# Performance work log

Hardware: AMD Instinct MI355X
Metric: run time of the kernel (lower is better)

## Reference

```python
import jax, jax.numpy as jnp
import numpy as np

NUM_HEADS = 16
EPS = 1e-05


def setup_inputs() -> dict:
    key = jax.random.key(0)
    k1, k2, k3 = jax.random.split(key, 3)
    b, n, d = 2, 2048, 1024
    x = jax.random.normal(k1, (b, n, d), dtype=jnp.float32)
    # nn.Linear weights stored here as (in, out); scaled like typical init
    wqkv = jax.random.normal(k2, (d, 3 * d), dtype=jnp.float32) * (1.0 / np.sqrt(d))
    wo = jax.random.normal(k3, (d, d), dtype=jnp.float32) * (1.0 / np.sqrt(d))
    return {"x": x, "wqkv": wqkv, "wo": wo}


def reference(x, wqkv, wo):
    b, n, d = x.shape
    h = NUM_HEADS
    hd = d // h
    qkv = x @ wqkv                      # (b, n, 3d)
    q, k, v = jnp.split(qkv, 3, axis=-1)
    q = jax.nn.relu(q)
    k = jax.nn.relu(k)
    # (b, n, h*hd) -> (b, h, n, hd)
    split_heads = lambda t: t.reshape(b, n, h, hd).transpose(0, 2, 1, 3)
    q, k, v = split_heads(q), split_heads(k), split_heads(v)
    # cumulative outer products: kv[b,h,t] = sum_{s<=t} k_s (x) v_s  -> (b,h,n,hd,hd)
    kv = jnp.cumsum(k[..., :, None] * v[..., None, :], axis=2)
    num = jnp.einsum('bhnd,bhnde->bhne', q, kv)          # (b, h, n, hd)
    k_sum = jnp.cumsum(k, axis=2)                        # (b, h, n, hd)
    den = jnp.einsum('bhnd,bhnd->bhn', q, k_sum)[..., None] + EPS
    y = num / den                                        # (b, h, n, hd)
    y = y.transpose(0, 2, 1, 3).reshape(b, n, d)         # merge heads
    return y @ wo
```

## Files before the change

kernel.cpp:

```cpp
#include <hip/hip_runtime.h>
#include <hip/hip_bf16.h>

#define SEQ    2048
#define DMODEL 1024
#define NHEADS 16
#define HD     64
#define CS     64
#define NC     (SEQ / CS)
#define STSZ   (HD * HD + HD)
#define EPS_LA 1e-5f
#define LP     72

typedef __attribute__((ext_vector_type(8))) short  bf16x8;
typedef __attribute__((ext_vector_type(8))) unsigned short ushort8;
typedef __attribute__((ext_vector_type(4))) float  f32x4;

__device__ __forceinline__ void gload_lds16(const void* g, void* l) {
  __builtin_amdgcn_global_load_lds(
      (const __attribute__((address_space(1))) void*)g,
      (__attribute__((address_space(3))) void*)l, 16, 0, 0);
}

__device__ __forceinline__ ushort f2bf(float x) {
  __hip_bfloat16 h = __float2bfloat16(x);
  return __builtin_bit_cast(ushort, h);
}
__device__ __forceinline__ float bf2f(ushort u) {
  unsigned int v = ((unsigned int)u) << 16;
  return __builtin_bit_cast(float, v);
}

__device__ __forceinline__ void transpose_tile(
    const float* __restrict__ src, ushort* __restrict__ dst,
    int R, int Ncols, int r0, int c0, float (*t)[65], int tid) {
  const int lr = tid >> 2;
  const int lc = (tid & 3) * 16;
  const float* sp = src + (size_t)(r0 + lr) * Ncols + c0 + lc;
  #pragma unroll
  for (int j = 0; j < 4; ++j) {
    float4 v = *(const float4*)(sp + j * 4);
    t[lr][lc + j * 4 + 0] = v.x;
    t[lr][lc + j * 4 + 1] = v.y;
    t[lr][lc + j * 4 + 2] = v.z;
    t[lr][lc + j * 4 + 3] = v.w;
  }
  __syncthreads();
  ushort out[16];
  #pragma unroll
  for (int j = 0; j < 16; ++j)
    out[j] = f2bf(t[lc + j][lr]);
  ushort* dp = dst + (size_t)(c0 + lr) * R + r0 + lc;
  *(uint4*)dp = *(const uint4*)&out[0];
  *(uint4*)(dp + 8) = *(const uint4*)&out[8];
}

__global__ __launch_bounds__(256) void prep(
    const float* __restrict__ x, const float* __restrict__ wqkv,
    const float* __restrict__ wo, ushort* __restrict__ xb,
    ushort* __restrict__ wqkvT, ushort* __restrict__ woT) {
  __shared__ float t[64][65];
  const int bid = blockIdx.x;
  const int tid = threadIdx.x;
  if (bid < 4096) {
    const int i = bid * 256 + tid;
    float4 v = *(const float4*)(x + (size_t)i * 4);
    ushort4 o;
    o.x = f2bf(v.x); o.y = f2bf(v.y); o.z = f2bf(v.z); o.w = f2bf(v.w);
    *(ushort4*)(xb + (size_t)i * 4) = o;
  } else if (bid < 4096 + 768) {
    const int b2 = bid - 4096;
    const int bx = b2 % 48, by = b2 / 48;
    transpose_tile(wqkv, wqkvT, DMODEL, 3 * DMODEL, by * 64, bx * 64, t, tid);
  } else {
    const int b3 = bid - 4096 - 768;
    const int bx = b3 % 16, by = b3 / 16;
    transpose_tile(wo, woT, DMODEL, DMODEL, by * 64, bx * 64, t, tid);
  }
}

template <bool OUT_BF16>
__global__ __launch_bounds__(256) void gemm_swz(
    const ushort* __restrict__ A, const ushort* __restrict__ Bt,
    void* __restrict__ Cv, int M, int N, int K, int relu_limit) {
  __shared__ ushort Asm[128 * 64];
  __shared__ ushort Bsm[128 * 64];

  const int tid  = threadIdx.x;
  const int lane = tid & 63;
  const int w    = tid >> 6;
  const int wr   = w >> 1, wc = w & 1;
  const int brow = blockIdx.y * 128;
  const int bcol = blockIdx.x * 128;

  f32x4 acc[4][4];
  #pragma unroll
  for (int i = 0; i < 4; ++i)
    #pragma unroll
    for (int j = 0; j < 4; ++j) acc[i][j] = (f32x4)0.f;

  const int r8   = lane >> 3;
  const int arow = w * 32 + r8;
  const int acol = ((lane & 7) ^ r8) * 8;
  const ushort* Ag = A  + (size_t)(brow + arow) * K + acol;
  const ushort* Bg = Bt + (size_t)(bcol + arow) * K + acol;

  const int l15 = lane & 15;
  const int khi = (lane >> 4) * 8;

  for (int k0 = 0; k0 < K; k0 += 64) {
    #pragma unroll
    for (int u = 0; u < 4; ++u) {
      gload_lds16(Ag + k0 + (size_t)u * 8 * K, &Asm[(w * 4 + u) * 512]);
      gload_lds16(Bg + k0 + (size_t)u * 8 * K, &Bsm[(w * 4 + u) * 512]);
    }
    __syncthreads();
    #pragma unroll
    for (int kk = 0; kk < 2; ++kk) {
      const int ko = kk * 32 + khi;
      bf16x8 af[4], bfr[4];
      #pragma unroll
      for (int mi = 0; mi < 4; ++mi) {
        const int row = wr * 64 + mi * 16 + l15;
        af[mi] = *(const bf16x8*)&Asm[row * 64 + (ko ^ ((row & 7) << 3))];
      }
      #pragma unroll
      for (int ni = 0; ni < 4; ++ni) {
        const int row = wc * 64 + ni * 16 + l15;
        bfr[ni] = *(const bf16x8*)&Bsm[row * 64 + (ko ^ ((row & 7) << 3))];
      }
      #pragma unroll
      for (int mi = 0; mi < 4; ++mi)
        #pragma unroll
        for (int ni = 0; ni < 4; ++ni)
          acc[mi][ni] = __builtin_amdgcn_mfma_f32_16x16x32_bf16(
              af[mi], bfr[ni], acc[mi][ni], 0, 0, 0);
    }
    __syncthreads();
  }

  #pragma unroll
  for (int mi = 0; mi < 4; ++mi) {
    #pragma unroll
    for (int ni = 0; ni < 4; ++ni) {
      const int r0  = brow + wr * 64 + mi * 16 + (lane >> 4) * 4;
      const int col = bcol + wc * 64 + ni * 16 + l15;
      const bool rl = col < relu_limit;
      #pragma unroll
      for (int i = 0; i < 4; ++i) {
        float v = acc[mi][ni][i];
        if (rl) v = fmaxf(v, 0.f);
        if (OUT_BF16)
          ((ushort*)Cv)[(size_t)(r0 + i) * N + col] = f2bf(v);
        else
          ((float*)Cv)[(size_t)(r0 + i) * N + col] = v;
      }
    }
  }
}

__global__ __launch_bounds__(256) void chunk_sums_mfma(
    const ushort* __restrict__ qkvb, ushort* __restrict__ state) {
  __shared__ ushort Kt[64 * LP];
  __shared__ ushort Vt[64 * LP];

  const int bh = blockIdx.x >> 5;
  const int c  = blockIdx.x & (NC - 1);
  const int b  = bh >> 4;
  const int h  = bh & (NHEADS - 1);
  const int tid = threadIdx.x;

  const size_t rs   = 3 * DMODEL;
  const size_t base = ((size_t)(b * SEQ + c * CS)) * rs + (size_t)h * HD;

  const int r  = tid >> 2;
  const int sg = (tid & 3) * 16;
  {
    const ushort* src = qkvb + base + (size_t)r * rs + sg;
    ushort8 k0 = *(const ushort8*)(src + DMODEL);
    ushort8 k1 = *(const ushort8*)(src + DMODEL + 8);
    ushort8 v0 = *(const ushort8*)(src + 2 * DMODEL);
    ushort8 v1 = *(const ushort8*)(src + 2 * DMODEL + 8);
    #pragma unroll
    for (int j = 0; j < 8; ++j) {
      Kt[(sg + j) * LP + r]     = k0[j];
      Kt[(sg + 8 + j) * LP + r] = k1[j];
      Vt[(sg + j) * LP + r]     = v0[j];
      Vt[(sg + 8 + j) * LP + r] = v1[j];
    }
  }
  __syncthreads();

  const int lane = tid & 63;
  const int w    = tid >> 6;
  const int l15  = lane & 15;
  const int khi  = (lane >> 4) * 8;

  bf16x8 va[2];
  #pragma unroll
  for (int kk = 0; kk < 2; ++kk)
    va[kk] = *(const bf16x8*)&Vt[(w * 16 + l15) * LP + kk * 32 + khi];

  f32x4 a[4];
  #pragma unroll
  for (int ct = 0; ct < 4; ++ct) {
    a[ct] = (f32x4)0.f;
    #pragma unroll
    for (int kk = 0; kk < 2; ++kk)
      a[ct] = __builtin_amdgcn_mfma_f32_16x16x32_bf16(
          va[kk], *(const bf16x8*)&Kt[(ct * 16 + l15) * LP + kk * 32 + khi],
          a[ct], 0, 0, 0);
  }

  ushort* st = state + (size_t)blockIdx.x * STSZ;
  #pragma unroll
  for (int ct = 0; ct < 4; ++ct) {
    #pragma unroll
    for (int i = 0; i < 4; ++i) {
      const int e = w * 16 + (lane >> 4) * 4 + i;
      const int d = ct * 16 + l15;
      st[e * HD + d] = f2bf(a[ct][i]);
    }
  }

  if (tid < HD) {
    float s = 0.f;
    #pragma unroll 8
    for (int t = 0; t < CS; ++t) s += bf2f(Kt[tid * LP + t]);
    st[HD * HD + tid] = f2bf(s);
  }
}

__global__ __launch_bounds__(256) void chunk_prefix(ushort* __restrict__ state) {
  const int g = blockIdx.x * 256 + threadIdx.x;
  const int total = 2 * NHEADS * STSZ;
  if (g >= total) return;
  const int bh   = g / STSZ;
  const int elem = g - bh * STSZ;
  ushort* p = state + (size_t)bh * NC * STSZ + elem;

  float run = 0.f;
  #pragma unroll
  for (int c = 0; c < NC; ++c) {
    const float t = bf2f(p[(size_t)c * STSZ]);
    p[(size_t)c * STSZ] = f2bf(run);
    run += t;
  }
}

__global__ __launch_bounds__(256) void chunk_out_mfma(
    const ushort* __restrict__ qkvb, const ushort* __restrict__ state,
    ushort* __restrict__ y) {
  __shared__ ushort Qs[64 * LP];
  __shared__ ushort Ks[64 * LP];
  __shared__ ushort Vt[80 * LP];
  __shared__ ushort Kv[80 * LP];
  __shared__ ushort Sm[64 * LP];

  const int bh = blockIdx.x >> 5;
  const int c  = blockIdx.x & (NC - 1);
  const int b  = bh >> 4;
  const int h  = bh & (NHEADS - 1);
  const int tid = threadIdx.x;

  const size_t rs   = 3 * DMODEL;
  const size_t base = ((size_t)(b * SEQ + c * CS)) * rs + (size_t)h * HD;

  {
    const int r  = tid >> 2;
    const int sg = (tid & 3) * 16;
    const ushort* src = qkvb + base + (size_t)r * rs + sg;
    ushort8 q0 = *(const ushort8*)(src);
    ushort8 q1 = *(const ushort8*)(src + 8);
    ushort8 k0 = *(const ushort8*)(src + DMODEL);
    ushort8 k1 = *(const ushort8*)(src + DMODEL + 8);
    ushort8 v0 = *(const ushort8*)(src + 2 * DMODEL);
    ushort8 v1 = *(const ushort8*)(src + 2 * DMODEL + 8);
    *(ushort8*)&Qs[r * LP + sg]     = q0;
    *(ushort8*)&Qs[r * LP + sg + 8] = q1;
    *(ushort8*)&Ks[r * LP + sg]     = k0;
    *(ushort8*)&Ks[r * LP + sg + 8] = k1;
    #pragma unroll
    for (int j = 0; j < 8; ++j) {
      Vt[(sg + j) * LP + r]     = v0[j];
      Vt[(sg + 8 + j) * LP + r] = v1[j];
    }
  }
  {
    const int idx = tid * 4;
    const int row = 64 + (idx >> 6);
    const int col = idx & 63;
    const ushort val = (row == 64) ? (ushort)0x3F80 : (ushort)0;
    ushort4 v4 = {val, val, val, val};
    *(ushort4*)&Vt[row * LP + col] = v4;
  }
  {
    const ushort* sp = state + ((size_t)bh * NC + c) * STSZ;
    const int off = tid * 16;
    const int e   = off >> 6;
    const int col = off & 63;
    *(ushort8*)&Kv[e * LP + col]     = *(const ushort8*)(sp + off);
    *(ushort8*)&Kv[e * LP + col + 8] = *(const ushort8*)(sp + off + 8);
    if (tid < 16) {
      const int c4 = tid * 4;
      *(ushort4*)&Kv[64 * LP + c4] = *(const ushort4*)(sp + HD * HD + c4);
    }
    if (tid < 240) {
      const int idx = tid * 4;
      const int row = 65 + (idx >> 6);
      const int col2 = idx & 63;
      ushort4 z = {0, 0, 0, 0};
      *(ushort4*)&Kv[row * LP + col2] = z;
    }
  }
  __syncthreads();

  const int lane = tid & 63;
  const int w    = tid >> 6;
  const int l15  = lane & 15;
  const int khi  = (lane >> 4) * 8;

  bf16x8 qa[2];
  #pragma unroll
  for (int kk = 0; kk < 2; ++kk)
    qa[kk] = *(const bf16x8*)&Qs[(w * 16 + l15) * LP + kk * 32 + khi];

  {
    f32x4 sac[4];
    #pragma unroll
    for (int ct = 0; ct < 4; ++ct) {
      sac[ct] = (f32x4)0.f;
      #pragma unroll
      for (int kk = 0; kk < 2; ++kk)
        sac[ct] = __builtin_amdgcn_mfma_f32_16x16x32_bf16(
            qa[kk], *(const bf16x8*)&Ks[(ct * 16 + l15) * LP + kk * 32 + khi],
            sac[ct], 0, 0, 0);
    }
    const int t0 = w * 16 + (lane >> 4) * 4;
    #pragma unroll
    for (int ct = 0; ct < 4; ++ct) {
      const int s = ct * 16 + l15;
      #pragma unroll
      for (int i = 0; i < 4; ++i) {
        const int t = t0 + i;
        const float v = (s <= t) ? sac[ct][i] : 0.f;
        Sm[t * LP + s] = f2bf(v);
      }
    }
  }
  __syncthreads();

  bf16x8 sa[2];
  #pragma unroll
  for (int kk = 0; kk < 2; ++kk)
    sa[kk] = *(const bf16x8*)&Sm[(w * 16 + l15) * LP + kk * 32 + khi];

  f32x4 o[5];
  #pragma unroll
  for (int ct = 0; ct < 5; ++ct) {
    o[ct] = (f32x4)0.f;
    #pragma unroll
    for (int kk = 0; kk < 2; ++kk)
      o[ct] = __builtin_amdgcn_mfma_f32_16x16x32_bf16(
          qa[kk], *(const bf16x8*)&Kv[(ct * 16 + l15) * LP + kk * 32 + khi],
          o[ct], 0, 0, 0);
    #pragma unroll
    for (int kk = 0; kk < 2; ++kk)
      o[ct] = __builtin_amdgcn_mfma_f32_16x16x32_bf16(
          sa[kk], *(const bf16x8*)&Vt[(ct * 16 + l15) * LP + kk * 32 + khi],
          o[ct], 0, 0, 0);
  }

  float den[4];
  #pragma unroll
  for (int i = 0; i < 4; ++i)
    den[i] = __shfl(o[4][i], lane & 48) + EPS_LA;

  const int t0 = w * 16 + (lane >> 4) * 4;
  #pragma unroll
  for (int ct = 0; ct < 4; ++ct) {
    const int e = ct * 16 + l15;
    #pragma unroll
    for (int i = 0; i < 4; ++i) {
      const int t = t0 + i;
      y[((size_t)(b * SEQ + c * CS + t)) * DMODEL + (size_t)h * HD + e] =
          f2bf(o[ct][i] / den[i]);
    }
  }
}

extern "C" void kernel_launch(void* const* d_in, const int* in_sizes, int n_in,
                              void* d_out, int out_size, void* d_ws,
                              size_t ws_size, hipStream_t stream) {
  (void)in_sizes; (void)n_in; (void)out_size; (void)ws_size;
  const float* x    = (const float*)d_in[0];
  const float* wqkv = (const float*)d_in[1];
  const float* wo   = (const float*)d_in[2];
  float* out = (float*)d_out;

  const int M  = 2 * SEQ;
  const int K  = DMODEL;
  const int N1 = 3 * DMODEL;
  const int N2 = DMODEL;

  ushort* stateb = (ushort*)d_ws;
  ushort* qkvb   = stateb + (size_t)2 * NHEADS * NC * STSZ;
  ushort* xb     = qkvb + (size_t)M * N1;
  ushort* yb     = xb + (size_t)M * K;
  ushort* wqkvT  = yb + (size_t)M * K;
  ushort* woT    = wqkvT + (size_t)K * N1;

  dim3 blk(256);

  prep<<<dim3(4096 + 768 + 256), blk, 0, stream>>>(x, wqkv, wo, xb, wqkvT, woT);

  gemm_swz<true><<<dim3(N1 / 128, M / 128), blk, 0, stream>>>(
      xb, wqkvT, qkvb, M, N1, K, 2 * DMODEL);

  chunk_sums_mfma<<<dim3(2 * NHEADS * NC), blk, 0, stream>>>(qkvb, stateb);

  const int total = 2 * NHEADS * STSZ;
  chunk_prefix<<<dim3((total + 255) / 256), blk, 0, stream>>>(stateb);

  chunk_out_mfma<<<dim3(2 * NHEADS * NC), blk, 0, stream>>>(qkvb, stateb, yb);

  gemm_swz<false><<<dim3(N2 / 128, M / 128), blk, 0, stream>>>(
      yb, woT, out, M, N2, K, 0);
}
```

Measured before the change: 90.08 us.

## Double-buffer GEMM LDS tiles with interleaved prefetch and XCD-aware block remap

Both GEMMs now use two LDS buffers: the next K-tile is loaded asynchronously while MFMAs run on the current one, so there is one block-wide sync per tile instead of a load-then-wait pattern. Issue is split into two phases with s_barrier and setprio around the MFMA bursts. The grid is flattened to 1D and remapped so neighbouring tiles land on the same XCD, aimed at L2 reuse. LDS per block doubles to 64KB, which may lower occupancy, and the remap assumes the block count divides by 8.

```diff
diff --git a/kernel.cpp b/kernel.cpp
--- a/kernel.cpp
+++ b/kernel.cpp
@@ -79,18 +79,24 @@
 }
 
 template <bool OUT_BF16>
-__global__ __launch_bounds__(256) void gemm_swz(
+__global__ __launch_bounds__(256) void gemm_ph(
     const ushort* __restrict__ A, const ushort* __restrict__ Bt,
-    void* __restrict__ Cv, int M, int N, int K, int relu_limit) {
-  __shared__ ushort Asm[128 * 64];
-  __shared__ ushort Bsm[128 * 64];
+    void* __restrict__ Cv, int M, int N, int K, int relu_limit, int nbx) {
+  __shared__ ushort Asm[2][128 * 64];
+  __shared__ ushort Bsm[2][128 * 64];
+
+  int wg = blockIdx.x;
+  const int cpx = gridDim.x >> 3;
+  wg = (wg & 7) * cpx + (wg >> 3);
+  const int bx = wg % nbx;
+  const int by = wg / nbx;
+  const int brow = by * 128;
+  const int bcol = bx * 128;
 
   const int tid  = threadIdx.x;
   const int lane = tid & 63;
   const int w    = tid >> 6;
   const int wr   = w >> 1, wc = w & 1;
-  const int brow = blockIdx.y * 128;
-  const int bcol = blockIdx.x * 128;
 
   f32x4 acc[4][4];
   #pragma unroll
@@ -107,35 +113,52 @@
   const int l15 = lane & 15;
   const int khi = (lane >> 4) * 8;
 
-  for (int k0 = 0; k0 < K; k0 += 64) {
-    #pragma unroll
-    for (int u = 0; u < 4; ++u) {
-      gload_lds16(Ag + k0 + (size_t)u * 8 * K, &Asm[(w * 4 + u) * 512]);
-      gload_lds16(Bg + k0 + (size_t)u * 8 * K, &Bsm[(w * 4 + u) * 512]);
-    }
-    __syncthreads();
-    #pragma unroll
-    for (int kk = 0; kk < 2; ++kk) {
-      const int ko = kk * 32 + khi;
+  #pragma unroll
+  for (int u = 0; u < 4; ++u) {
+    gload_lds16(Ag + (size_t)u * 8 * K, &Asm[0][(w * 4 + u) * 512]);
+    gload_lds16(Bg + (size_t)u * 8 * K, &Bsm[0][(w * 4 + u) * 512]);
+  }
+  __syncthreads();
+
+  const int NT = K >> 6;
+  int cur = 0;
+  for (int kt = 0; kt < NT; ++kt) {
+    const ushort* An = Ag + (size_t)(kt + 1) * 64;
+    const ushort* Bn = Bg + (size_t)(kt + 1) * 64;
+    const bool pf = (kt + 1 < NT);
+    #pragma unroll
+    for (int ph = 0; ph < 2; ++ph) {
+      const int ko = ph * 32 + khi;
       bf16x8 af[4], bfr[4];
       #pragma unroll
       for (int mi = 0; mi < 4; ++mi) {
         const int row = wr * 64 + mi * 16 + l15;
-        af[mi] = *(const bf16x8*)&Asm[row * 64 + (ko ^ ((row & 7) << 3))];
+        af[mi] = *(const bf16x8*)&Asm[cur][row * 64 + (ko ^ ((row & 7) << 3))];
       }
       #pragma unroll
       for (int ni = 0; ni < 4; ++ni) {
         const int row = wc * 64 + ni * 16 + l15;
-        bfr[ni] = *(const bf16x8*)&Bsm[row * 64 + (ko ^ ((row & 7) << 3))];
+        bfr[ni] = *(const bf16x8*)&Bsm[cur][row * 64 + (ko ^ ((row & 7) << 3))];
       }
+      if (pf) {
+        #pragma unroll
+        for (int u = ph * 2; u < ph * 2 + 2; ++u) {
+          gload_lds16(An + (size_t)u * 8 * K, &Asm[cur ^ 1][(w * 4 + u) * 512]);
+          gload_lds16(Bn + (size_t)u * 8 * K, &Bsm[cur ^ 1][(w * 4 + u) * 512]);
+        }
+      }
+      __builtin_amdgcn_s_barrier();
+      __builtin_amdgcn_s_setprio(1);
       #pragma unroll
       for (int mi = 0; mi < 4; ++mi)
         #pragma unroll
         for (int ni = 0; ni < 4; ++ni)
           acc[mi][ni] = __builtin_amdgcn_mfma_f32_16x16x32_bf16(
               af[mi], bfr[ni], acc[mi][ni], 0, 0, 0);
+      __builtin_amdgcn_s_setprio(0);
     }
     __syncthreads();
+    cur ^= 1;
   }
 
   #pragma unroll
@@ -413,8 +436,8 @@
 
   prep<<<dim3(4096 + 768 + 256), blk, 0, stream>>>(x, wqkv, wo, xb, wqkvT, woT);
 
-  gemm_swz<true><<<dim3(N1 / 128, M / 128), blk, 0, stream>>>(
-      xb, wqkvT, qkvb, M, N1, K, 2 * DMODEL);
+  gemm_ph<true><<<dim3((N1 / 128) * (M / 128)), blk, 0, stream>>>(
+      xb, wqkvT, qkvb, M, N1, K, 2 * DMODEL, N1 / 128);
 
   chunk_sums_mfma<<<dim3(2 * NHEADS * NC), blk, 0, stream>>>(qkvb, stateb);
 
@@ -423,6 +446,6 @@
 
   chunk_out_mfma<<<dim3(2 * NHEADS * NC), blk, 0, stream>>>(qkvb, stateb, yb);
 
-  gemm_swz<false><<<dim3(N2 / 128, M / 128), blk, 0, stream>>>(
-      yb, woT, out, M, N2, K, 0);
-}
+  gemm_ph<false><<<dim3((N2 / 128) * (M / 128)), blk, 0, stream>>>(
+      yb, woT, out, M, N2, K, 0, N2 / 128);
+}
```

New measurement: 88.99 us. About the same (-1.2%).

## Double-buffer GEMM LDS tiles with vmcnt-based prefetch of next K tile

Applied to the files above, without the earlier changes.

Converts both bf16 GEMMs to a double-buffered LDS pipeline: the next K tile is issued via global_load_lds into the alternate buffer before computing on the current one, and a partial s_waitcnt vmcnt(8) waits only for the current tile. Raw s_barrier plus sched_barrier replaces __syncthreads, so one barrier pair per iteration guards both buffers. The aim is to hide global-load latency behind the MFMA work. It doubles LDS use to 64 KB per block, which may lower occupancy, and correctness depends on the hand-written vmcnt counts matching the issued loads.

```diff
diff --git a/kernel.cpp b/kernel.cpp
--- a/kernel.cpp
+++ b/kernel.cpp
@@ -79,11 +79,11 @@
 }
 
 template <bool OUT_BF16>
-__global__ __launch_bounds__(256) void gemm_swz(
+__global__ __launch_bounds__(256) void gemm_cnt(
     const ushort* __restrict__ A, const ushort* __restrict__ Bt,
     void* __restrict__ Cv, int M, int N, int K, int relu_limit) {
-  __shared__ ushort Asm[128 * 64];
-  __shared__ ushort Bsm[128 * 64];
+  __shared__ ushort Asm[2][128 * 64];
+  __shared__ ushort Bsm[2][128 * 64];
 
   const int tid  = threadIdx.x;
   const int lane = tid & 63;
@@ -107,13 +107,34 @@
   const int l15 = lane & 15;
   const int khi = (lane >> 4) * 8;
 
-  for (int k0 = 0; k0 < K; k0 += 64) {
-    #pragma unroll
-    for (int u = 0; u < 4; ++u) {
-      gload_lds16(Ag + k0 + (size_t)u * 8 * K, &Asm[(w * 4 + u) * 512]);
-      gload_lds16(Bg + k0 + (size_t)u * 8 * K, &Bsm[(w * 4 + u) * 512]);
-    }
-    __syncthreads();
+  #pragma unroll
+  for (int u = 0; u < 4; ++u) {
+    gload_lds16(Ag + (size_t)u * 8 * K, &Asm[0][(w * 4 + u) * 512]);
+    gload_lds16(Bg + (size_t)u * 8 * K, &Bsm[0][(w * 4 + u) * 512]);
+  }
+
+  const int NT = K >> 6;
+  int cur = 0;
+  for (int kt = 0; kt < NT; ++kt) {
+    __builtin_amdgcn_s_barrier();
+    __builtin_amdgcn_sched_barrier(0);
+    if (kt + 1 < NT) {
+      const ushort* An = Ag + (size_t)(kt + 1) * 64;
+      const ushort* Bn = Bg + (size_t)(kt + 1) * 64;
+      const int nxt = cur ^ 1;
+      #pragma unroll
+      for (int u = 0; u < 4; ++u) {
+        gload_lds16(An + (size_t)u * 8 * K, &Asm[nxt][(w * 4 + u) * 512]);
+        gload_lds16(Bn + (size_t)u * 8 * K, &Bsm[nxt][(w * 4 + u) * 512]);
+      }
+      asm volatile("s_waitcnt vmcnt(8)" ::: "memory");
+    } else {
+      asm volatile("s_waitcnt vmcnt(0)" ::: "memory");
+    }
+    __builtin_amdgcn_sched_barrier(0);
+    __builtin_amdgcn_s_barrier();
+    __builtin_amdgcn_sched_barrier(0);
+
     #pragma unroll
     for (int kk = 0; kk < 2; ++kk) {
       const int ko = kk * 32 + khi;
@@ -121,12 +142,12 @@
       #pragma unroll
       for (int mi = 0; mi < 4; ++mi) {
         const int row = wr * 64 + mi * 16 + l15;
-        af[mi] = *(const bf16x8*)&Asm[row * 64 + (ko ^ ((row & 7) << 3))];
+        af[mi] = *(const bf16x8*)&Asm[cur][row * 64 + (ko ^ ((row & 7) << 3))];
       }
       #pragma unroll
       for (int ni = 0; ni < 4; ++ni) {
         const int row = wc * 64 + ni * 16 + l15;
-        bfr[ni] = *(const bf16x8*)&Bsm[row * 64 + (ko ^ ((row & 7) << 3))];
+        bfr[ni] = *(const bf16x8*)&Bsm[cur][row * 64 + (ko ^ ((row & 7) << 3))];
       }
       #pragma unroll
       for (int mi = 0; mi < 4; ++mi)
@@ -135,7 +156,7 @@
           acc[mi][ni] = __builtin_amdgcn_mfma_f32_16x16x32_bf16(
               af[mi], bfr[ni], acc[mi][ni], 0, 0, 0);
     }
-    __syncthreads();
+    cur ^= 1;
   }
 
   #pragma unroll
@@ -413,7 +434,7 @@
 
   prep<<<dim3(4096 + 768 + 256), blk, 0, stream>>>(x, wqkv, wo, xb, wqkvT, woT);
 
-  gemm_swz<true><<<dim3(N1 / 128, M / 128), blk, 0, stream>>>(
+  gemm_cnt<true><<<dim3(N1 / 128, M / 128), blk, 0, stream>>>(
       xb, wqkvT, qkvb, M, N1, K, 2 * DMODEL);
 
   chunk_sums_mfma<<<dim3(2 * NHEADS * NC), blk, 0, stream>>>(qkvb, stateb);
@@ -423,6 +444,6 @@
 
   chunk_out_mfma<<<dim3(2 * NHEADS * NC), blk, 0, stream>>>(qkvb, stateb, yb);
 
-  gemm_swz<false><<<dim3(N2 / 128, M / 128), blk, 0, stream>>>(
+  gemm_cnt<false><<<dim3(N2 / 128, M / 128), blk, 0, stream>>>(
       yb, woT, out, M, N2, K, 0);
 }
```

After: 94.01 us. 4.4% more time.
